# Kernel tuning notes

Hardware: AMD Instinct MI355X
Metric: run time of the kernel (lower is better)

The kernel has to match this reference:

```python
import jax, jax.numpy as jnp
import numpy as np

NU, NM = 100000, 20000
E, EUU = 1000000, 500000
DU, DM, H = 64, 128, 128
BN_EPS = 1e-5


def _sage(x_src, x_dst, src, dst, Wl, bl, Wr):
    # PyG SAGEConv (mean aggr): lin_l(mean_j x_src[j]) + lin_r(x_dst)
    n_dst = x_dst.shape[0]
    msg = x_src[src]                                   # [E, H] gather
    agg = jax.ops.segment_sum(msg, dst, num_segments=n_dst)
    cnt = jax.ops.segment_sum(jnp.ones((dst.shape[0],), x_src.dtype), dst, num_segments=n_dst)
    agg = agg / jnp.maximum(cnt, 1.0)[:, None]
    return agg @ Wl + bl + x_dst @ Wr


def setup_inputs() -> dict:
    key = jax.random.key(0)
    ks = iter(jax.random.split(key, 40))
    s = 0.08  # weight scale for numerical stability
    d = {}
    d['user_feat'] = jax.random.normal(next(ks), (NU, DU), jnp.float32)
    d['movie_feat'] = jax.random.normal(next(ks), (NM, DM), jnp.float32)
    d['W_user'] = jax.random.normal(next(ks), (DU, H), jnp.float32) * s
    d['b_user'] = jnp.zeros((H,), jnp.float32)
    d['W_movie'] = jax.random.normal(next(ks), (DM, H), jnp.float32) * s
    d['b_movie'] = jnp.zeros((H,), jnp.float32)
    for name in ['u2m1', 'm2u1', 'u2m2', 'm2u2', 'u2u']:
        d[name + '_Wl'] = jax.random.normal(next(ks), (H, H), jnp.float32) * s
        d[name + '_bl'] = jnp.zeros((H,), jnp.float32)
        d[name + '_Wr'] = jax.random.normal(next(ks), (H, H), jnp.float32) * s
    d['p1_W'] = jax.random.normal(next(ks), (2 * H, H), jnp.float32) * s
    d['p1_b'] = jnp.zeros((H,), jnp.float32)
    d['bn_gamma'] = jnp.ones((H,), jnp.float32)
    d['bn_beta'] = jnp.zeros((H,), jnp.float32)
    d['bn_mean'] = jnp.zeros((H,), jnp.float32)
    d['bn_var'] = jax.random.uniform(next(ks), (H,), jnp.float32, 0.5, 1.5)
    d['p2_W'] = jax.random.normal(next(ks), (H, 1), jnp.float32) * s
    d['p2_b'] = jnp.zeros((1,), jnp.float32)
    d['rated_src'] = jax.random.randint(next(ks), (E,), 0, NU, jnp.int32)
    d['rated_dst'] = jax.random.randint(next(ks), (E,), 0, NM, jnp.int32)
    d['uu_src'] = jax.random.randint(next(ks), (EUU,), 0, NU, jnp.int32)
    d['uu_dst'] = jax.random.randint(next(ks), (EUU,), 0, NU, jnp.int32)
    return d


def reference(user_feat, movie_feat, W_user, b_user, W_movie, b_movie,
              u2m1_Wl, u2m1_bl, u2m1_Wr, m2u1_Wl, m2u1_bl, m2u1_Wr,
              u2m2_Wl, u2m2_bl, u2m2_Wr, m2u2_Wl, m2u2_bl, m2u2_Wr,
              u2u_Wl, u2u_bl, u2u_Wr,
              p1_W, p1_b, bn_gamma, bn_beta, bn_mean, bn_var, p2_W, p2_b,
              rated_src, rated_dst, uu_src, uu_dst):
    relu = jax.nn.relu
    ux = relu(user_feat @ W_user + b_user)     # [NU, H]
    mx = relu(movie_feat @ W_movie + b_movie)  # [NM, H]
    # user -> movie, movie -> user (reversed edges), twice
    mx = relu(_sage(ux, mx, rated_src, rated_dst, u2m1_Wl, u2m1_bl, u2m1_Wr))
    ux = relu(_sage(mx, ux, rated_dst, rated_src, m2u1_Wl, m2u1_bl, m2u1_Wr))
    mx = relu(_sage(ux, mx, rated_src, rated_dst, u2m2_Wl, u2m2_bl, u2m2_Wr))
    ux = relu(_sage(mx, ux, rated_dst, rated_src, m2u2_Wl, m2u2_bl, m2u2_Wr))
    # user -> user follows
    ux = relu(_sage(ux, ux, uu_src, uu_dst, u2u_Wl, u2u_bl, u2u_Wr))
    # edge embedding + MLP predictor (BN/Dropout in eval mode)
    emb = jnp.concatenate([ux[rated_src], mx[rated_dst]], axis=1)  # [E, 2H]
    h = emb @ p1_W + p1_b
    h = (h - bn_mean) * jax.lax.rsqrt(bn_var + BN_EPS) * bn_gamma + bn_beta
    h = relu(h)
    pred = jax.nn.sigmoid(h @ p2_W + p2_b)[:, 0]
    return pred * 4.0 + 1.0
```

## Files before the change

### kernel.cpp

```cpp
#include <hip/hip_runtime.h>
#include <cmath>


#define NUSR 100000
#define NMOV 20000
#define NEDG 1000000
#define NEUU 500000
#define DH 128

#define CAPM 96
#define CAPU 32
#define CAPUU 24

#define NBD 128
#define WD 157
#define NBS 128
#define WS 782
#define NBU 196
#define WU 512
#define NBT (NBD + NBS + NBU)

#define LCD 36
#define LCS 36
#define LCU 20
#define BKD 8448
#define BKS 8448
#define BKU 2944

#define NBINB 977
#define EPSL 32
#define NEPB (EPSL * 128)

#define GLU ((NUSR + 127) / 128)
#define GLM ((NMOV + 127) / 128)
#define GSU 512
#define GSM 157

typedef unsigned short ushort_t;
typedef unsigned char uchar_t;
typedef __attribute__((ext_vector_type(8))) short short8;
typedef __attribute__((ext_vector_type(4))) float f32x4;
typedef __attribute__((ext_vector_type(2))) float f32x2;

__device__ __forceinline__ ushort_t f2bf(float f) {
  unsigned u = __float_as_uint(f);
  u += 0x7FFFu + ((u >> 16) & 1u);
  return (ushort_t)(u >> 16);
}
__device__ __forceinline__ uchar_t f2fp8(float v) {
  return (uchar_t)(__builtin_amdgcn_cvt_pk_fp8_f32(v, v, 0, false) & 0xFF);
}
__device__ __forceinline__ void fp8x8_to_f32(uint2 v, float* f) {
  f32x2 a = __builtin_amdgcn_cvt_pk_f32_fp8((int)v.x, false);
  f32x2 b = __builtin_amdgcn_cvt_pk_f32_fp8((int)v.x, true);
  f32x2 c = __builtin_amdgcn_cvt_pk_f32_fp8((int)v.y, false);
  f32x2 d = __builtin_amdgcn_cvt_pk_f32_fp8((int)v.y, true);
  f[0] = a.x; f[1] = a.y; f[2] = b.x; f[3] = b.y;
  f[4] = c.x; f[5] = c.y; f[6] = d.x; f[7] = d.y;
}
__device__ __forceinline__ int ntl(const int* p) { return __builtin_nontemporal_load(p); }
__device__ __forceinline__ unsigned ntl(const unsigned* p) { return __builtin_nontemporal_load(p); }
__device__ __forceinline__ ushort_t ntl(const ushort_t* p) { return __builtin_nontemporal_load(p); }

struct PrepArgs {
  const float* Wl[6];
  const float* Wr[6];
};
__global__ __launch_bounds__(256) void prep_all_k(
    PrepArgs pa, ushort_t* __restrict__ Wt,
    const float* __restrict__ W_user, const float* __restrict__ W_movie,
    ushort_t* __restrict__ WtU, ushort_t* __restrict__ WtM,
    const float* __restrict__ p1b, const float* __restrict__ gamma,
    const float* __restrict__ beta, const float* __restrict__ mean,
    const float* __restrict__ var,
    float* __restrict__ SEP, float* __restrict__ TEP,
    int* __restrict__ bcnt)
{
  int blk = blockIdx.x;
  if (blk < 768) {
    int wi = blk >> 7;
    int idx = (blk & 127) * 256 + threadIdx.x;
    int n = idx >> 8, k = idx & 255;
    const float* Wl = pa.Wl[wi];
    const float* Wr = pa.Wr[wi];
    float v = (k < DH) ? Wl[k * DH + n] : Wr[(k - DH) * DH + n];
    Wt[(size_t)wi * 32768 + n * 256 + k] = f2bf(v);
  } else if (blk < 800) {
    int idx = (blk - 768) * 256 + threadIdx.x;
    int n = idx >> 6, k = idx & 63;
    WtU[n * 64 + k] = f2bf(W_user[k * DH + n]);
  } else if (blk < 864) {
    int idx = (blk - 800) * 256 + threadIdx.x;
    int n = idx >> 7, k = idx & 127;
    WtM[n * 128 + k] = f2bf(W_movie[k * DH + n]);
  } else {
    int f = threadIdx.x;
    if (f < DH) {
      float sc = gamma[f] * rsqrtf(var[f] + 1e-5f);
      SEP[f] = sc;
      TEP[f] = (p1b[f] - mean[f]) * sc + beta[f];
    }
    for (int i = threadIdx.x; i < NBT; i += 256) bcnt[i] = 0;
  }
}

__global__ __launch_bounds__(256) void bin_rated_k(
    const int* __restrict__ rsrc, const int* __restrict__ rdst,
    unsigned* __restrict__ bkt_d, uint2* __restrict__ bkt_s2,
    int* __restrict__ bcnt)
{
  __shared__ unsigned sb_d[NBD * LCD];
  __shared__ uint2 sb_s[NBS * LCS];
  __shared__ int lcnt[NBD + NBS];
  __shared__ int gbase[NBD + NBS];
  const int tid = threadIdx.x;
  for (int i = tid; i < NBD + NBS; i += 256) lcnt[i] = 0;
  __syncthreads();
  const int c = blockIdx.x;
#pragma unroll
  for (int it = 0; it < 4; ++it) {
    int e = c * 1024 + it * 256 + tid;
    if (e < NEDG) {
      int s = ntl(&rsrc[e]), d = ntl(&rdst[e]);
      int bd = d / WD;
      int o = atomicAdd(&lcnt[bd], 1);
      if (o < LCD) sb_d[bd * LCD + o] = (unsigned)(d - bd * WD) | ((unsigned)s << 8);
      int bs = s / WS;
      int o2 = atomicAdd(&lcnt[NBD + bs], 1);
      if (o2 < LCS)
        sb_s[bs * LCS + o2] =
            make_uint2((unsigned)(s - bs * WS) | ((unsigned)d << 10), (unsigned)e);
    }
  }
  __syncthreads();
  for (int i = tid; i < NBD + NBS; i += 256) {
    int n = lcnt[i];
    if (n > LCD) n = LCD;
    lcnt[i] = n;
    gbase[i] = atomicAdd(&bcnt[i], n);
  }
  __syncthreads();
  const int qw = tid >> 4, lq = tid & 15;
  for (int t = qw; t < NBD + NBS; t += 16) {
    int n = lcnt[t], gb = gbase[t];
    if (t < NBD) {
      if (gb + n > BKD) n = BKD - gb;
      unsigned* gp = bkt_d + (size_t)t * BKD;
      const unsigned* sp = sb_d + t * LCD;
      for (int i = lq; i < n; i += 16) gp[gb + i] = sp[i];
    } else {
      int b = t - NBD;
      if (gb + n > BKS) n = BKS - gb;
      uint2* gp = bkt_s2 + (size_t)b * BKS;
      const uint2* sp = sb_s + b * LCS;
      for (int i = lq; i < n; i += 16) gp[gb + i] = sp[i];
    }
  }
}

__global__ __launch_bounds__(256) void bin_uu_k(
    const int* __restrict__ usrc, const int* __restrict__ udst,
    unsigned* __restrict__ bkt_u, int* __restrict__ bcnt)
{
  __shared__ unsigned sb_u[NBU * LCU];
  __shared__ int lcnt[NBU];
  __shared__ int gbase[NBU];
  const int tid = threadIdx.x;
  for (int i = tid; i < NBU; i += 256) lcnt[i] = 0;
  __syncthreads();
  const int c = blockIdx.x;
#pragma unroll
  for (int it = 0; it < 2; ++it) {
    int e = c * 512 + it * 256 + tid;
    if (e < NEUU) {
      int s = ntl(&usrc[e]), d = ntl(&udst[e]);
      int bu = d >> 9;
      int o = atomicAdd(&lcnt[bu], 1);
      if (o < LCU) sb_u[bu * LCU + o] = (unsigned)(d & 511) | ((unsigned)s << 9);
    }
  }
  __syncthreads();
  for (int i = tid; i < NBU; i += 256) {
    int n = lcnt[i];
    if (n > LCU) n = LCU;
    lcnt[i] = n;
    gbase[i] = atomicAdd(&bcnt[NBD + NBS + i], n);
  }
  __syncthreads();
  const int qw = tid >> 4, lq = tid & 15;
  for (int t = qw; t < NBU; t += 16) {
    int n = lcnt[t], gb = gbase[t];
    if (gb + n > BKU) n = BKU - gb;
    unsigned* gp = bkt_u + (size_t)t * BKU;
    const unsigned* sp = sb_u + t * LCU;
    for (int i = lq; i < n; i += 16) gp[gb + i] = sp[i];
  }
}

__global__ __launch_bounds__(256) void csr_k(
    const unsigned* __restrict__ bkt_d, const uint2* __restrict__ bkt_s2,
    const unsigned* __restrict__ bkt_u, const int* __restrict__ bcnt,
    int* __restrict__ cnt_m, int* __restrict__ cnt_u, int* __restrict__ cnt_uu,
    int* __restrict__ col_m, ushort_t* __restrict__ col_u, int* __restrict__ col_uu)
{
  __shared__ int lc[WS];
  __shared__ alignas(16) unsigned cbuf[WD * CAPM];
  const int tid = threadIdx.x;
  const int bid = blockIdx.x;
  if (bid < NBD) {
    const int b = bid;
    const int nr = (NMOV - b * WD < WD) ? (NMOV - b * WD) : WD;
    for (int m = tid; m < nr; m += 256) lc[m] = 0;
    __syncthreads();
    int n = bcnt[b]; if (n > BKD) n = BKD;
    const unsigned* B = bkt_d + (size_t)b * BKD;
    for (int i = tid; i < n; i += 256) {
      unsigned v = ntl(&B[i]);
      int m = (int)(v & 255u);
      int o = atomicAdd(&lc[m], 1);
      if (o < CAPM) cbuf[m * CAPM + o] = v >> 8;
    }
    __syncthreads();
    for (int m = tid; m < nr; m += 256) cnt_m[b * WD + m] = lc[m];
    int4* dst = (int4*)(col_m + (size_t)b * WD * CAPM);
    const int4* src = (const int4*)cbuf;
    const int tot = nr * (CAPM / 4);
    for (int i = tid; i < tot; i += 256) dst[i] = src[i];
  } else if (bid < NBD + NBS) {
    const int b = bid - NBD;
    const int nr = (NUSR - b * WS < WS) ? (NUSR - b * WS) : WS;
    for (int u = tid; u < nr; u += 256) lc[u] = 0;
    __syncthreads();
    int n = bcnt[NBD + b]; if (n > BKS) n = BKS;
    const uint2* B = bkt_s2 + (size_t)b * BKS;
    ushort_t* cb16 = (ushort_t*)cbuf;
    for (int i = tid; i < n; i += 256) {
      unsigned v = B[i].x;
      int u = (int)(v & 1023u);
      int o = atomicAdd(&lc[u], 1);
      if (o < CAPU) cb16[u * CAPU + o] = (ushort_t)(v >> 10);
    }
    __syncthreads();
    for (int u = tid; u < nr; u += 256) cnt_u[b * WS + u] = lc[u];
    int4* dst = (int4*)(col_u + (size_t)b * WS * CAPU);
    const int4* src = (const int4*)cbuf;
    const int tot = nr * (CAPU / 8);
    for (int i = tid; i < tot; i += 256) dst[i] = src[i];
  } else {
    const int b = bid - NBD - NBS;
    const int nr = (NUSR - b * WU < WU) ? (NUSR - b * WU) : WU;
    for (int u = tid; u < nr; u += 256) lc[u] = 0;
    __syncthreads();
    int n = bcnt[NBD + NBS + b]; if (n > BKU) n = BKU;
    const unsigned* B = bkt_u + (size_t)b * BKU;
    for (int i = tid; i < n; i += 256) {
      unsigned v = ntl(&B[i]);
      int u = (int)(v & 511u);
      int o = atomicAdd(&lc[u], 1);
      if (o < CAPUU) cbuf[u * CAPUU + o] = v >> 9;
    }
    __syncthreads();
    for (int u = tid; u < nr; u += 256) cnt_uu[b * WU + u] = lc[u];
    int4* dst = (int4*)(col_uu + (size_t)b * WU * CAPUU);
    const int4* src = (const int4*)cbuf;
    const int tot = nr * (CAPUU / 4);
    for (int i = tid; i < tot; i += 256) dst[i] = src[i];
  }
}

template <int K>
__device__ __forceinline__ void lin_body(
    int lblk, const float* __restrict__ X, const ushort_t* __restrict__ Wt,
    const float* __restrict__ b, ushort_t* __restrict__ Y,
    uchar_t* __restrict__ Y8, int N)
{
  const int wave = threadIdx.x >> 6;
  const int lane = threadIdx.x & 63;
  const int row0 = (lblk * 4 + wave) * 32;
  if (row0 >= N) return;
  const int lm = lane & 15;
  const int koff = (lane >> 4) * 8;

  f32x4 acc[2][8];
#pragma unroll
  for (int a = 0; a < 2; ++a)
#pragma unroll
    for (int nt = 0; nt < 8; ++nt) acc[a][nt] = (f32x4){0.f, 0.f, 0.f, 0.f};

#pragma unroll
  for (int ks = 0; ks < K / 32; ++ks) {
    short8 af[2];
#pragma unroll
    for (int a = 0; a < 2; ++a) {
      const float* p = X + (size_t)(row0 + a * 16 + lm) * K + ks * 32 + koff;
      float4 v0 = *(const float4*)p;
      float4 v1 = *(const float4*)(p + 4);
      short8 s;
      s[0] = (short)f2bf(v0.x); s[1] = (short)f2bf(v0.y);
      s[2] = (short)f2bf(v0.z); s[3] = (short)f2bf(v0.w);
      s[4] = (short)f2bf(v1.x); s[5] = (short)f2bf(v1.y);
      s[6] = (short)f2bf(v1.z); s[7] = (short)f2bf(v1.w);
      af[a] = s;
    }
#pragma unroll
    for (int nt = 0; nt < 8; ++nt) {
      short8 bf = *(const short8*)&Wt[(nt * 16 + lm) * K + ks * 32 + koff];
      acc[0][nt] = __builtin_amdgcn_mfma_f32_16x16x32_bf16(af[0], bf, acc[0][nt], 0, 0, 0);
      acc[1][nt] = __builtin_amdgcn_mfma_f32_16x16x32_bf16(af[1], bf, acc[1][nt], 0, 0, 0);
    }
  }

  const int quad = lane >> 4;
  float bv[8];
#pragma unroll
  for (int nt = 0; nt < 8; ++nt) bv[nt] = b[nt * 16 + lm];
#pragma unroll
  for (int a = 0; a < 2; ++a) {
#pragma unroll
    for (int reg = 0; reg < 4; ++reg) {
      const int r = row0 + a * 16 + quad * 4 + reg;
      float vv[8];
#pragma unroll
      for (int nt = 0; nt < 8; ++nt)
        vv[nt] = fmaxf(acc[a][nt][reg] + bv[nt], 0.f);
#pragma unroll
      for (int nt = 0; nt < 8; ++nt)
        Y[(size_t)r * DH + nt * 16 + lm] = f2bf(vv[nt]);
#pragma unroll
      for (int nt = 0; nt < 8; ++nt)
        Y8[(size_t)r * DH + nt * 16 + lm] = f2fp8(vv[nt]);
    }
  }
}

__global__ __launch_bounds__(256) void lin2_k(
    const float* __restrict__ user_feat, const ushort_t* __restrict__ WtU,
    const float* __restrict__ b_user, ushort_t* __restrict__ ux, uchar_t* __restrict__ ux8,
    const float* __restrict__ movie_feat, const ushort_t* __restrict__ WtM,
    const float* __restrict__ b_movie, ushort_t* __restrict__ mx, uchar_t* __restrict__ mx8)
{
  const int blk = blockIdx.x;
  if (blk < GLU) lin_body<64>(blk, user_feat, WtU, b_user, ux, ux8, NUSR);
  else lin_body<128>(blk - GLU, movie_feat, WtM, b_movie, mx, mx8, NMOV);
}

template <typename CT, int CAP, int UNR>
__global__ __launch_bounds__(256) void agg_mean4_k(
    const uchar_t* __restrict__ x8, const int* __restrict__ cnt,
    const CT* __restrict__ col, ushort_t* __restrict__ out, int N)
{
  const int wave = threadIdx.x >> 6;
  const int lane = threadIdx.x & 63;
  const int lm = lane & 15, q = lane >> 4;
  const int row = blockIdx.x * 16 + wave * 4 + q;
  if (row >= N) return;
  const int deg = cnt[row];
  const int e = (deg < CAP) ? deg : CAP;
  const CT* crow = col + (size_t)row * CAP;
  float a[8];
#pragma unroll
  for (int j = 0; j < 8; ++j) a[j] = 0.f;
  int i = 0;
  if (UNR >= 16) {
    for (; i + 15 < e; i += 16) {
      uint2 v[16];
#pragma unroll
      for (int u = 0; u < 16; ++u) {
        int s = (int)ntl(&crow[i + u]);
        v[u] = *(const uint2*)(x8 + (size_t)s * DH + lm * 8);
      }
#pragma unroll
      for (int u = 0; u < 16; ++u) {
        float f0[8];
        fp8x8_to_f32(v[u], f0);
#pragma unroll
        for (int j = 0; j < 8; ++j) a[j] += f0[j];
      }
    }
  }
  if (UNR >= 8) {
    for (; i + 7 < e; i += 8) {
      uint2 v[8];
#pragma unroll
      for (int u = 0; u < 8; ++u) {
        int s = (int)ntl(&crow[i + u]);
        v[u] = *(const uint2*)(x8 + (size_t)s * DH + lm * 8);
      }
#pragma unroll
      for (int u = 0; u < 8; ++u) {
        float f0[8];
        fp8x8_to_f32(v[u], f0);
#pragma unroll
        for (int j = 0; j < 8; ++j) a[j] += f0[j];
      }
    }
  }
  for (; i + 3 < e; i += 4) {
    uint2 v0, v1, v2, v3;
    int s0 = (int)ntl(&crow[i]), s1 = (int)ntl(&crow[i + 1]);
    int s2 = (int)ntl(&crow[i + 2]), s3 = (int)ntl(&crow[i + 3]);
    v0 = *(const uint2*)(x8 + (size_t)s0 * DH + lm * 8);
    v1 = *(const uint2*)(x8 + (size_t)s1 * DH + lm * 8);
    v2 = *(const uint2*)(x8 + (size_t)s2 * DH + lm * 8);
    v3 = *(const uint2*)(x8 + (size_t)s3 * DH + lm * 8);
    float f0[8], f1[8], f2[8], f3[8];
    fp8x8_to_f32(v0, f0); fp8x8_to_f32(v1, f1);
    fp8x8_to_f32(v2, f2); fp8x8_to_f32(v3, f3);
#pragma unroll
    for (int j = 0; j < 8; ++j) a[j] += (f0[j] + f1[j]) + (f2[j] + f3[j]);
  }
  for (; i < e; ++i) {
    uint2 v0 = *(const uint2*)(x8 + (size_t)(int)ntl(&crow[i]) * DH + lm * 8);
    float f0[8];
    fp8x8_to_f32(v0, f0);
#pragma unroll
    for (int j = 0; j < 8; ++j) a[j] += f0[j];
  }
  float inv = 1.f / (float)(deg > 1 ? deg : 1);
  unsigned p0 = f2bf(a[0] * inv) | ((unsigned)f2bf(a[1] * inv) << 16);
  unsigned p1 = f2bf(a[2] * inv) | ((unsigned)f2bf(a[3] * inv) << 16);
  unsigned p2 = f2bf(a[4] * inv) | ((unsigned)f2bf(a[5] * inv) << 16);
  unsigned p3 = f2bf(a[6] * inv) | ((unsigned)f2bf(a[7] * inv) << 16);
  *(int4*)(out + (size_t)row * DH + lm * 8) = make_int4(p0, p1, p2, p3);
}

__global__ __launch_bounds__(256) void sage_mfma_k(
    const ushort_t* __restrict__ A0, const ushort_t* __restrict__ A1,
    const ushort_t* __restrict__ Wt, const float* __restrict__ bl,
    ushort_t* __restrict__ out, uchar_t* __restrict__ out8, int N)
{
  __shared__ alignas(16) ushort_t WtS[32768];
  const int tid = threadIdx.x;
  for (int f = tid; f < 4096; f += 256) {
    const int r = f >> 5, c = f & 31;
    const int4 v = *(const int4*)(Wt + (size_t)f * 8);
    *(int4*)&WtS[(size_t)((r << 5) | (c ^ (r & 31))) << 3] = v;
  }
  __syncthreads();

  const int wave = tid >> 6;
  const int lane = tid & 63;
  const int lm = lane & 15;
  const int kq = lane >> 4;
  const int koff = kq * 8;
  const int quad = kq;

  float bv[8];
#pragma unroll
  for (int nt = 0; nt < 8; ++nt) bv[nt] = bl[nt * 16 + lm];

  const int T = (N + 31) >> 5;
  for (int t = (int)blockIdx.x * 4 + wave; t < T; t += (int)gridDim.x * 4) {
    const int row0 = t * 32;
    size_t abase[2];
#pragma unroll
    for (int a = 0; a < 2; ++a) abase[a] = (size_t)(row0 + a * 16 + lm) * DH;

    f32x4 acc[2][8];
#pragma unroll
    for (int a = 0; a < 2; ++a)
#pragma unroll
      for (int nt = 0; nt < 8; ++nt) acc[a][nt] = (f32x4){0.f, 0.f, 0.f, 0.f};

#pragma unroll
    for (int ks = 0; ks < 8; ++ks) {
      short8 af[2];
#pragma unroll
      for (int a = 0; a < 2; ++a) {
        const ushort_t* p = (ks < 4) ? (A0 + abase[a] + ks * 32 + koff)
                                     : (A1 + abase[a] + (ks - 4) * 32 + koff);
        af[a] = *(const short8*)p;
      }
#pragma unroll
      for (int nt = 0; nt < 8; ++nt) {
        const int r = nt * 16 + lm;
        const int c = (ks * 4 + kq) ^ (r & 31);
        short8 bf = *(const short8*)&WtS[(size_t)((r << 5) | c) << 3];
        acc[0][nt] = __builtin_amdgcn_mfma_f32_16x16x32_bf16(af[0], bf, acc[0][nt], 0, 0, 0);
        acc[1][nt] = __builtin_amdgcn_mfma_f32_16x16x32_bf16(af[1], bf, acc[1][nt], 0, 0, 0);
      }
    }

#pragma unroll
    for (int a = 0; a < 2; ++a) {
#pragma unroll
      for (int reg = 0; reg < 4; ++reg) {
        const int r = row0 + a * 16 + quad * 4 + reg;
        float vv[8];
#pragma unroll
        for (int nt = 0; nt < 8; ++nt)
          vv[nt] = fmaxf(acc[a][nt][reg] + bv[nt], 0.f);
#pragma unroll
        for (int nt = 0; nt < 8; ++nt)
          out[(size_t)r * DH + nt * 16 + lm] = f2bf(vv[nt]);
        if (out8) {
#pragma unroll
          for (int nt = 0; nt < 8; ++nt)
            out8[(size_t)r * DH + nt * 16 + lm] = f2fp8(vv[nt]);
        }
      }
    }
  }
}

__device__ __forceinline__ void proj_body(
    int lblk, const ushort_t* __restrict__ A, const ushort_t* __restrict__ Wt,
    int kofs, ushort_t* __restrict__ out, int N)
{
  const int wave = threadIdx.x >> 6;
  const int lane = threadIdx.x & 63;
  const int row0 = (lblk * 4 + wave) * 32;
  if (row0 >= N) return;
  const int lm = lane & 15;
  const int koff = (lane >> 4) * 8;

  size_t abase[2];
#pragma unroll
  for (int a = 0; a < 2; ++a) abase[a] = (size_t)(row0 + a * 16 + lm) * DH;

  f32x4 acc[2][8];
#pragma unroll
  for (int a = 0; a < 2; ++a)
#pragma unroll
    for (int nt = 0; nt < 8; ++nt) acc[a][nt] = (f32x4){0.f, 0.f, 0.f, 0.f};

#pragma unroll
  for (int ks = 0; ks < 4; ++ks) {
    short8 af[2];
#pragma unroll
    for (int a = 0; a < 2; ++a) af[a] = *(const short8*)(A + abase[a] + ks * 32 + koff);
#pragma unroll
    for (int nt = 0; nt < 8; ++nt) {
      short8 bf = *(const short8*)&Wt[(nt * 16 + lm) * 256 + kofs + ks * 32 + koff];
      acc[0][nt] = __builtin_amdgcn_mfma_f32_16x16x32_bf16(af[0], bf, acc[0][nt], 0, 0, 0);
      acc[1][nt] = __builtin_amdgcn_mfma_f32_16x16x32_bf16(af[1], bf, acc[1][nt], 0, 0, 0);
    }
  }

  const int quad = lane >> 4;
#pragma unroll
  for (int a = 0; a < 2; ++a) {
#pragma unroll
    for (int reg = 0; reg < 4; ++reg) {
      const int r = row0 + a * 16 + quad * 4 + reg;
#pragma unroll
      for (int nt = 0; nt < 8; ++nt)
        out[(size_t)r * DH + nt * 16 + lm] = f2bf(acc[a][nt][reg]);
    }
  }
}

__global__ __launch_bounds__(256) void proj2_k(
    const ushort_t* __restrict__ ux, const ushort_t* __restrict__ mx,
    const ushort_t* __restrict__ Wt, ushort_t* __restrict__ pu,
    ushort_t* __restrict__ pm, int gmU)
{
  if ((int)blockIdx.x < gmU) proj_body(blockIdx.x, ux, Wt, 0, pu, NUSR);
  else proj_body(blockIdx.x - gmU, mx, Wt, DH, pm, NMOV);
}

__global__ __launch_bounds__(256) void ep_bkt_k(
    const ushort_t* __restrict__ pu, const ushort_t* __restrict__ pm,
    const uint2* __restrict__ bkt_s2, const int* __restrict__ bcnt,
    const float* __restrict__ SEP, const float* __restrict__ TEP,
    const float* __restrict__ p2W, const float* __restrict__ p2b,
    float* __restrict__ out)
{
  const int b = (int)blockIdx.x & 127;
  const int sl = (int)blockIdx.x >> 7;
  const int tid = threadIdx.x;
  const int lm = tid & 15;
  const int qw = tid >> 4;
  const int f0 = lm * 8;

  float S[8], T8[8], w2[8];
#pragma unroll
  for (int j = 0; j < 8; ++j) {
    S[j] = SEP[f0 + j];
    T8[j] = TEP[f0 + j];
    w2[j] = p2W[f0 + j];
  }
  const float bias2 = p2b[0];

  int n = bcnt[NBD + b];
  if (n > BKS) n = BKS;
  const uint2* B = bkt_s2 + (size_t)b * BKS;
  const int ub = b * WS;
  const int chunk = (n + EPSL - 1) / EPSL;
  const int st = sl * chunk;
  int en = st + chunk;
  if (en > n) en = n;

  for (int i = st + qw; i < en; i += 32) {
    const int i2 = i + 16;
    const bool v2 = (i2 < en);
    uint2 e0 = B[i];
    uint2 e1 = v2 ? B[i2] : e0;
    int s0 = ub + (int)(e0.x & 1023u), d0 = (int)(e0.x >> 10);
    int s1 = ub + (int)(e1.x & 1023u), d1 = (int)(e1.x >> 10);
    int4 uv0 = *(const int4*)(pu + (s0 << 7) + f0);
    int4 mv0 = *(const int4*)(pm + (d0 << 7) + f0);
    int4 uv1 = *(const int4*)(pu + (s1 << 7) + f0);
    int4 mv1 = *(const int4*)(pm + (d1 << 7) + f0);
    float fu0[8], fm0[8], fu1[8], fm1[8];
    {
      unsigned a0 = (unsigned)uv0.x, b0 = (unsigned)uv0.y, c0 = (unsigned)uv0.z, dd0 = (unsigned)uv0.w;
      fu0[0] = __uint_as_float(a0 << 16); fu0[1] = __uint_as_float(a0 & 0xFFFF0000u);
      fu0[2] = __uint_as_float(b0 << 16); fu0[3] = __uint_as_float(b0 & 0xFFFF0000u);
      fu0[4] = __uint_as_float(c0 << 16); fu0[5] = __uint_as_float(c0 & 0xFFFF0000u);
      fu0[6] = __uint_as_float(dd0 << 16); fu0[7] = __uint_as_float(dd0 & 0xFFFF0000u);
      unsigned a1 = (unsigned)mv0.x, b1 = (unsigned)mv0.y, c1 = (unsigned)mv0.z, dd1 = (unsigned)mv0.w;
      fm0[0] = __uint_as_float(a1 << 16); fm0[1] = __uint_as_float(a1 & 0xFFFF0000u);
      fm0[2] = __uint_as_float(b1 << 16); fm0[3] = __uint_as_float(b1 & 0xFFFF0000u);
      fm0[4] = __uint_as_float(c1 << 16); fm0[5] = __uint_as_float(c1 & 0xFFFF0000u);
      fm0[6] = __uint_as_float(dd1 << 16); fm0[7] = __uint_as_float(dd1 & 0xFFFF0000u);
      unsigned a2 = (unsigned)uv1.x, b2 = (unsigned)uv1.y, c2 = (unsigned)uv1.z, dd2 = (unsigned)uv1.w;
      fu1[0] = __uint_as_float(a2 << 16); fu1[1] = __uint_as_float(a2 & 0xFFFF0000u);
      fu1[2] = __uint_as_float(b2 << 16); fu1[3] = __uint_as_float(b2 & 0xFFFF0000u);
      fu1[4] = __uint_as_float(c2 << 16); fu1[5] = __uint_as_float(c2 & 0xFFFF0000u);
      fu1[6] = __uint_as_float(dd2 << 16); fu1[7] = __uint_as_float(dd2 & 0xFFFF0000u);
      unsigned a3 = (unsigned)mv1.x, b3 = (unsigned)mv1.y, c3 = (unsigned)mv1.z, dd3 = (unsigned)mv1.w;
      fm1[0] = __uint_as_float(a3 << 16); fm1[1] = __uint_as_float(a3 & 0xFFFF0000u);
      fm1[2] = __uint_as_float(b3 << 16); fm1[3] = __uint_as_float(b3 & 0xFFFF0000u);
      fm1[4] = __uint_as_float(c3 << 16); fm1[5] = __uint_as_float(c3 & 0xFFFF0000u);
      fm1[6] = __uint_as_float(dd3 << 16); fm1[7] = __uint_as_float(dd3 & 0xFFFF0000u);
    }
    float p0 = 0.f, p1 = 0.f;
#pragma unroll
    for (int j = 0; j < 8; ++j) {
      float h0 = fmaxf(fmaf(fu0[j] + fm0[j], S[j], T8[j]), 0.f);
      p0 = fmaf(h0, w2[j], p0);
      float h1 = fmaxf(fmaf(fu1[j] + fm1[j], S[j], T8[j]), 0.f);
      p1 = fmaf(h1, w2[j], p1);
    }
    p0 += __shfl_xor(p0, 1, 16);
    p0 += __shfl_xor(p0, 2, 16);
    p0 += __shfl_xor(p0, 4, 16);
    p0 += __shfl_xor(p0, 8, 16);
    p1 += __shfl_xor(p1, 1, 16);
    p1 += __shfl_xor(p1, 2, 16);
    p1 += __shfl_xor(p1, 4, 16);
    p1 += __shfl_xor(p1, 8, 16);
    if (lm == 0) {
      __builtin_nontemporal_store(4.f / (1.f + expf(-(p0 + bias2))) + 1.f, &out[e0.y]);
      if (v2)
        __builtin_nontemporal_store(4.f / (1.f + expf(-(p1 + bias2))) + 1.f, &out[e1.y]);
    }
  }
}

extern "C" void kernel_launch(void* const* d_in, const int* in_sizes, int n_in,
                              void* d_out, int out_size, void* d_ws, size_t ws_size,
                              hipStream_t stream)
{
  const float* user_feat = (const float*)d_in[0];
  const float* movie_feat = (const float*)d_in[1];
  const float* W_user = (const float*)d_in[2];
  const float* b_user = (const float*)d_in[3];
  const float* W_movie = (const float*)d_in[4];
  const float* b_movie = (const float*)d_in[5];
  const float* u2m1_Wl = (const float*)d_in[6];
  const float* u2m1_bl = (const float*)d_in[7];
  const float* u2m1_Wr = (const float*)d_in[8];
  const float* m2u1_Wl = (const float*)d_in[9];
  const float* m2u1_bl = (const float*)d_in[10];
  const float* m2u1_Wr = (const float*)d_in[11];
  const float* u2m2_Wl = (const float*)d_in[12];
  const float* u2m2_bl = (const float*)d_in[13];
  const float* u2m2_Wr = (const float*)d_in[14];
  const float* m2u2_Wl = (const float*)d_in[15];
  const float* m2u2_bl = (const float*)d_in[16];
  const float* m2u2_Wr = (const float*)d_in[17];
  const float* u2u_Wl = (const float*)d_in[18];
  const float* u2u_bl = (const float*)d_in[19];
  const float* u2u_Wr = (const float*)d_in[20];
  const float* p1_W = (const float*)d_in[21];
  const float* p1_b = (const float*)d_in[22];
  const float* bn_gamma = (const float*)d_in[23];
  const float* bn_beta = (const float*)d_in[24];
  const float* bn_mean = (const float*)d_in[25];
  const float* bn_var = (const float*)d_in[26];
  const float* p2_W = (const float*)d_in[27];
  const float* p2_b = (const float*)d_in[28];
  const int* rated_src = (const int*)d_in[29];
  const int* rated_dst = (const int*)d_in[30];
  const int* uu_src = (const int*)d_in[31];
  const int* uu_dst = (const int*)d_in[32];

  ushort_t* ux = (ushort_t*)d_ws;
  ushort_t* mx = ux + (size_t)NUSR * DH;
  ushort_t* agg = mx + (size_t)NMOV * DH;
  ushort_t* pm = agg + (size_t)NUSR * DH;
  ushort_t* Wt = pm + (size_t)NMOV * DH;
  ushort_t* WtU = Wt + 6 * 32768;
  ushort_t* WtM = WtU + 8192;
  float* SEP = (float*)(WtM + 16384);
  float* TEP = SEP + DH;
  int* col_m = (int*)(TEP + DH);
  ushort_t* col_u = (ushort_t*)(col_m + (size_t)NMOV * CAPM);
  int* col_uu = (int*)(col_u + (size_t)NUSR * CAPU);
  int* cntbuf = col_uu + (size_t)NUSR * CAPUU;
  uchar_t* ux8 = (uchar_t*)(cntbuf + (NMOV + 2 * NUSR + NBT));
  uchar_t* mx8 = ux8 + (size_t)NUSR * DH;
  uint2* bkt_s2 = (uint2*)(mx8 + (size_t)NMOV * DH);
  int* cnt_m = cntbuf;
  int* cnt_u = cntbuf + NMOV;
  int* cnt_uu = cntbuf + NMOV + NUSR;
  int* bcnt = cntbuf + NMOV + 2 * NUSR;

  unsigned* bkt_d = (unsigned*)agg;
  unsigned* bkt_u = bkt_d + (size_t)NBD * BKD;

  ushort_t* Wt_u2m1 = Wt + 0 * 32768;
  ushort_t* Wt_m2u1 = Wt + 1 * 32768;
  ushort_t* Wt_u2m2 = Wt + 2 * 32768;
  ushort_t* Wt_m2u2 = Wt + 3 * 32768;
  ushort_t* Wt_u2u  = Wt + 4 * 32768;
  ushort_t* Wt_p1   = Wt + 5 * 32768;
  ushort_t* pu = agg;

  PrepArgs pa;
  pa.Wl[0] = u2m1_Wl; pa.Wr[0] = u2m1_Wr;
  pa.Wl[1] = m2u1_Wl; pa.Wr[1] = m2u1_Wr;
  pa.Wl[2] = u2m2_Wl; pa.Wr[2] = u2m2_Wr;
  pa.Wl[3] = m2u2_Wl; pa.Wr[3] = m2u2_Wr;
  pa.Wl[4] = u2u_Wl;  pa.Wr[4] = u2u_Wr;
  pa.Wl[5] = p1_W;    pa.Wr[5] = p1_W + DH * DH;
  prep_all_k<<<865, 256, 0, stream>>>(
      pa, Wt, W_user, W_movie, WtU, WtM,
      p1_b, bn_gamma, bn_beta, bn_mean, bn_var, SEP, TEP, bcnt);

  bin_rated_k<<<NBINB, 256, 0, stream>>>(
      rated_src, rated_dst, bkt_d, bkt_s2, bcnt);
  bin_uu_k<<<NBINB, 256, 0, stream>>>(uu_src, uu_dst, bkt_u, bcnt);
  csr_k<<<NBT, 256, 0, stream>>>(
      bkt_d, bkt_s2, bkt_u, bcnt, cnt_m, cnt_u, cnt_uu, col_m, col_u, col_uu);
  lin2_k<<<GLU + GLM, 256, 0, stream>>>(
      user_feat, WtU, b_user, ux, ux8, movie_feat, WtM, b_movie, mx, mx8);

  const int gaM = (NMOV + 15) / 16, gaU = (NUSR + 15) / 16;
  agg_mean4_k<int, CAPM, 16><<<gaM, 256, 0, stream>>>(ux8, cnt_m, col_m, agg, NMOV);
  sage_mfma_k<<<GSM, 256, 0, stream>>>(agg, mx, Wt_u2m1, u2m1_bl, mx, mx8, NMOV);
  agg_mean4_k<ushort_t, CAPU, 8><<<gaU, 256, 0, stream>>>(mx8, cnt_u, col_u, agg, NUSR);
  sage_mfma_k<<<GSU, 256, 0, stream>>>(agg, ux, Wt_m2u1, m2u1_bl, ux, ux8, NUSR);
  agg_mean4_k<int, CAPM, 16><<<gaM, 256, 0, stream>>>(ux8, cnt_m, col_m, agg, NMOV);
  sage_mfma_k<<<GSM, 256, 0, stream>>>(agg, mx, Wt_u2m2, u2m2_bl, mx, mx8, NMOV);
  agg_mean4_k<ushort_t, CAPU, 8><<<gaU, 256, 0, stream>>>(mx8, cnt_u, col_u, agg, NUSR);
  sage_mfma_k<<<GSU, 256, 0, stream>>>(agg, ux, Wt_m2u2, m2u2_bl, ux, ux8, NUSR);
  agg_mean4_k<int, CAPUU, 8><<<gaU, 256, 0, stream>>>(ux8, cnt_uu, col_uu, agg, NUSR);
  sage_mfma_k<<<GSU, 256, 0, stream>>>(agg, ux, Wt_u2u, u2u_bl, ux, (uchar_t*)nullptr, NUSR);

  const int gmU = (NUSR + 127) / 128, gmM = (NMOV + 127) / 128;
  proj2_k<<<gmU + gmM, 256, 0, stream>>>(ux, mx, Wt_p1, pu, pm, gmU);
  ep_bkt_k<<<NEPB, 256, 0, stream>>>(
      pu, pm, bkt_s2, bcnt, SEP, TEP, p2_W, p2_b, (float*)d_out);
}
```

Before: 560.4 us.

## Fuse mean aggregation into SAGE MFMA kernel, removing intermediate agg buffer

Replaces the separate neighbor-mean gather kernel and the dense MFMA kernel with one kernel. Each wave gathers the fp8 neighbor rows for 16 destination rows, builds the bf16 A-fragment in registers, and multiplies it against the LDS-resident weights together with the self features. This removes the bf16 agg write and re-read plus one launch per layer. The trade-off is less gather parallelism, since each wave now handles 16 rows and each lane walks one row's edge list serially. That can cause load imbalance and fewer in-flight loads, especially for high-degree movie rows.

```diff
diff --git a/kernel.cpp b/kernel.cpp
--- a/kernel.cpp
+++ b/kernel.cpp
@@ -33,8 +33,8 @@
 
 #define GLU ((NUSR + 127) / 128)
 #define GLM ((NMOV + 127) / 128)
-#define GSU 512
-#define GSM 157
+#define GFU 512
+#define GFM 313
 
 typedef unsigned short ushort_t;
 typedef unsigned char uchar_t;
@@ -344,88 +344,10 @@
   else lin_body<128>(blk - GLU, movie_feat, WtM, b_movie, mx, mx8, NMOV);
 }
 
-template <typename CT, int CAP, int UNR>
-__global__ __launch_bounds__(256) void agg_mean4_k(
+template <typename CT, int CAP>
+__global__ __launch_bounds__(256) void fused_sage_k(
     const uchar_t* __restrict__ x8, const int* __restrict__ cnt,
-    const CT* __restrict__ col, ushort_t* __restrict__ out, int N)
-{
-  const int wave = threadIdx.x >> 6;
-  const int lane = threadIdx.x & 63;
-  const int lm = lane & 15, q = lane >> 4;
-  const int row = blockIdx.x * 16 + wave * 4 + q;
-  if (row >= N) return;
-  const int deg = cnt[row];
-  const int e = (deg < CAP) ? deg : CAP;
-  const CT* crow = col + (size_t)row * CAP;
-  float a[8];
-#pragma unroll
-  for (int j = 0; j < 8; ++j) a[j] = 0.f;
-  int i = 0;
-  if (UNR >= 16) {
-    for (; i + 15 < e; i += 16) {
-      uint2 v[16];
-#pragma unroll
-      for (int u = 0; u < 16; ++u) {
-        int s = (int)ntl(&crow[i + u]);
-        v[u] = *(const uint2*)(x8 + (size_t)s * DH + lm * 8);
-      }
-#pragma unroll
-      for (int u = 0; u < 16; ++u) {
-        float f0[8];
-        fp8x8_to_f32(v[u], f0);
-#pragma unroll
-        for (int j = 0; j < 8; ++j) a[j] += f0[j];
-      }
-    }
-  }
-  if (UNR >= 8) {
-    for (; i + 7 < e; i += 8) {
-      uint2 v[8];
-#pragma unroll
-      for (int u = 0; u < 8; ++u) {
-        int s = (int)ntl(&crow[i + u]);
-        v[u] = *(const uint2*)(x8 + (size_t)s * DH + lm * 8);
-      }
-#pragma unroll
-      for (int u = 0; u < 8; ++u) {
-        float f0[8];
-        fp8x8_to_f32(v[u], f0);
-#pragma unroll
-        for (int j = 0; j < 8; ++j) a[j] += f0[j];
-      }
-    }
-  }
-  for (; i + 3 < e; i += 4) {
-    uint2 v0, v1, v2, v3;
-    int s0 = (int)ntl(&crow[i]), s1 = (int)ntl(&crow[i + 1]);
-    int s2 = (int)ntl(&crow[i + 2]), s3 = (int)ntl(&crow[i + 3]);
-    v0 = *(const uint2*)(x8 + (size_t)s0 * DH + lm * 8);
-    v1 = *(const uint2*)(x8 + (size_t)s1 * DH + lm * 8);
-    v2 = *(const uint2*)(x8 + (size_t)s2 * DH + lm * 8);
-    v3 = *(const uint2*)(x8 + (size_t)s3 * DH + lm * 8);
-    float f0[8], f1[8], f2[8], f3[8];
-    fp8x8_to_f32(v0, f0); fp8x8_to_f32(v1, f1);
-    fp8x8_to_f32(v2, f2); fp8x8_to_f32(v3, f3);
-#pragma unroll
-    for (int j = 0; j < 8; ++j) a[j] += (f0[j] + f1[j]) + (f2[j] + f3[j]);
-  }
-  for (; i < e; ++i) {
-    uint2 v0 = *(const uint2*)(x8 + (size_t)(int)ntl(&crow[i]) * DH + lm * 8);
-    float f0[8];
-    fp8x8_to_f32(v0, f0);
-#pragma unroll
-    for (int j = 0; j < 8; ++j) a[j] += f0[j];
-  }
-  float inv = 1.f / (float)(deg > 1 ? deg : 1);
-  unsigned p0 = f2bf(a[0] * inv) | ((unsigned)f2bf(a[1] * inv) << 16);
-  unsigned p1 = f2bf(a[2] * inv) | ((unsigned)f2bf(a[3] * inv) << 16);
-  unsigned p2 = f2bf(a[4] * inv) | ((unsigned)f2bf(a[5] * inv) << 16);
-  unsigned p3 = f2bf(a[6] * inv) | ((unsigned)f2bf(a[7] * inv) << 16);
-  *(int4*)(out + (size_t)row * DH + lm * 8) = make_int4(p0, p1, p2, p3);
-}
-
-__global__ __launch_bounds__(256) void sage_mfma_k(
-    const ushort_t* __restrict__ A0, const ushort_t* __restrict__ A1,
+    const CT* __restrict__ col, const ushort_t* __restrict__ A1,
     const ushort_t* __restrict__ Wt, const float* __restrict__ bl,
     ushort_t* __restrict__ out, uchar_t* __restrict__ out8, int N)
 {
@@ -442,62 +364,112 @@
   const int lane = tid & 63;
   const int lm = lane & 15;
   const int kq = lane >> 4;
-  const int koff = kq * 8;
-  const int quad = kq;
 
   float bv[8];
 #pragma unroll
   for (int nt = 0; nt < 8; ++nt) bv[nt] = bl[nt * 16 + lm];
 
-  const int T = (N + 31) >> 5;
+  const int T = N >> 4;
   for (int t = (int)blockIdx.x * 4 + wave; t < T; t += (int)gridDim.x * 4) {
-    const int row0 = t * 32;
-    size_t abase[2];
-#pragma unroll
-    for (int a = 0; a < 2; ++a) abase[a] = (size_t)(row0 + a * 16 + lm) * DH;
-
-    f32x4 acc[2][8];
-#pragma unroll
-    for (int a = 0; a < 2; ++a)
-#pragma unroll
-      for (int nt = 0; nt < 8; ++nt) acc[a][nt] = (f32x4){0.f, 0.f, 0.f, 0.f};
-
-#pragma unroll
-    for (int ks = 0; ks < 8; ++ks) {
-      short8 af[2];
-#pragma unroll
-      for (int a = 0; a < 2; ++a) {
-        const ushort_t* p = (ks < 4) ? (A0 + abase[a] + ks * 32 + koff)
-                                     : (A1 + abase[a] + (ks - 4) * 32 + koff);
-        af[a] = *(const short8*)p;
+    const int row = t * 16 + lm;
+    const int deg = cnt[row];
+    const int e = (deg < CAP) ? deg : CAP;
+    const CT* crow = col + (size_t)row * CAP;
+    const uchar_t* xb = x8 + kq * 8;
+
+    float ac[4][8];
+#pragma unroll
+    for (int ks = 0; ks < 4; ++ks)
+#pragma unroll
+      for (int j = 0; j < 8; ++j) ac[ks][j] = 0.f;
+
+    int i = 0;
+    for (; i + 3 < e; i += 4) {
+      int s0 = (int)ntl(&crow[i]);
+      int s1 = (int)ntl(&crow[i + 1]);
+      int s2 = (int)ntl(&crow[i + 2]);
+      int s3 = (int)ntl(&crow[i + 3]);
+      uint2 v0[4], v1[4], v2[4], v3[4];
+#pragma unroll
+      for (int ks = 0; ks < 4; ++ks) {
+        v0[ks] = *(const uint2*)(xb + (size_t)s0 * DH + ks * 32);
+        v1[ks] = *(const uint2*)(xb + (size_t)s1 * DH + ks * 32);
+        v2[ks] = *(const uint2*)(xb + (size_t)s2 * DH + ks * 32);
+        v3[ks] = *(const uint2*)(xb + (size_t)s3 * DH + ks * 32);
       }
+#pragma unroll
+      for (int ks = 0; ks < 4; ++ks) {
+        float f0[8], f1[8], f2[8], f3[8];
+        fp8x8_to_f32(v0[ks], f0); fp8x8_to_f32(v1[ks], f1);
+        fp8x8_to_f32(v2[ks], f2); fp8x8_to_f32(v3[ks], f3);
+#pragma unroll
+        for (int j = 0; j < 8; ++j)
+          ac[ks][j] += (f0[j] + f1[j]) + (f2[j] + f3[j]);
+      }
+    }
+    for (; i < e; ++i) {
+      int s = (int)ntl(&crow[i]);
+#pragma unroll
+      for (int ks = 0; ks < 4; ++ks) {
+        uint2 v = *(const uint2*)(xb + (size_t)s * DH + ks * 32);
+        float f[8];
+        fp8x8_to_f32(v, f);
+#pragma unroll
+        for (int j = 0; j < 8; ++j) ac[ks][j] += f[j];
+      }
+    }
+
+    const float inv = 1.f / (float)(deg > 1 ? deg : 1);
+    short8 af[4];
+#pragma unroll
+    for (int ks = 0; ks < 4; ++ks) {
+      short8 s;
+#pragma unroll
+      for (int j = 0; j < 8; ++j) s[j] = (short)f2bf(ac[ks][j] * inv);
+      af[ks] = s;
+    }
+
+    f32x4 acc[8];
+#pragma unroll
+    for (int nt = 0; nt < 8; ++nt) acc[nt] = (f32x4){0.f, 0.f, 0.f, 0.f};
+
+#pragma unroll
+    for (int ks = 0; ks < 4; ++ks) {
 #pragma unroll
       for (int nt = 0; nt < 8; ++nt) {
         const int r = nt * 16 + lm;
         const int c = (ks * 4 + kq) ^ (r & 31);
         short8 bf = *(const short8*)&WtS[(size_t)((r << 5) | c) << 3];
-        acc[0][nt] = __builtin_amdgcn_mfma_f32_16x16x32_bf16(af[0], bf, acc[0][nt], 0, 0, 0);
-        acc[1][nt] = __builtin_amdgcn_mfma_f32_16x16x32_bf16(af[1], bf, acc[1][nt], 0, 0, 0);
+        acc[nt] = __builtin_amdgcn_mfma_f32_16x16x32_bf16(af[ks], bf, acc[nt], 0, 0, 0);
       }
     }
-
-#pragma unroll
-    for (int a = 0; a < 2; ++a) {
-#pragma unroll
-      for (int reg = 0; reg < 4; ++reg) {
-        const int r = row0 + a * 16 + quad * 4 + reg;
-        float vv[8];
+    const ushort_t* a1p = A1 + (size_t)row * DH + kq * 8;
+#pragma unroll
+    for (int ks = 4; ks < 8; ++ks) {
+      short8 afu = *(const short8*)(a1p + (ks - 4) * 32);
+#pragma unroll
+      for (int nt = 0; nt < 8; ++nt) {
+        const int r = nt * 16 + lm;
+        const int c = (ks * 4 + kq) ^ (r & 31);
+        short8 bf = *(const short8*)&WtS[(size_t)((r << 5) | c) << 3];
+        acc[nt] = __builtin_amdgcn_mfma_f32_16x16x32_bf16(afu, bf, acc[nt], 0, 0, 0);
+      }
+    }
+
+#pragma unroll
+    for (int reg = 0; reg < 4; ++reg) {
+      const int r = t * 16 + kq * 4 + reg;
+      float vv[8];
+#pragma unroll
+      for (int nt = 0; nt < 8; ++nt)
+        vv[nt] = fmaxf(acc[nt][reg] + bv[nt], 0.f);
+#pragma unroll
+      for (int nt = 0; nt < 8; ++nt)
+        out[(size_t)r * DH + nt * 16 + lm] = f2bf(vv[nt]);
+      if (out8) {
 #pragma unroll
         for (int nt = 0; nt < 8; ++nt)
-          vv[nt] = fmaxf(acc[a][nt][reg] + bv[nt], 0.f);
-#pragma unroll
-        for (int nt = 0; nt < 8; ++nt)
-          out[(size_t)r * DH + nt * 16 + lm] = f2bf(vv[nt]);
-        if (out8) {
-#pragma unroll
-          for (int nt = 0; nt < 8; ++nt)
-            out8[(size_t)r * DH + nt * 16 + lm] = f2fp8(vv[nt]);
-        }
+          out8[(size_t)r * DH + nt * 16 + lm] = f2fp8(vv[nt]);
       }
     }
   }
@@ -738,17 +710,16 @@
   lin2_k<<<GLU + GLM, 256, 0, stream>>>(
       user_feat, WtU, b_user, ux, ux8, movie_feat, WtM, b_movie, mx, mx8);
 
-  const int gaM = (NMOV + 15) / 16, gaU = (NUSR + 15) / 16;
-  agg_mean4_k<int, CAPM, 16><<<gaM, 256, 0, stream>>>(ux8, cnt_m, col_m, agg, NMOV);
-  sage_mfma_k<<<GSM, 256, 0, stream>>>(agg, mx, Wt_u2m1, u2m1_bl, mx, mx8, NMOV);
-  agg_mean4_k<ushort_t, CAPU, 8><<<gaU, 256, 0, stream>>>(mx8, cnt_u, col_u, agg, NUSR);
-  sage_mfma_k<<<GSU, 256, 0, stream>>>(agg, ux, Wt_m2u1, m2u1_bl, ux, ux8, NUSR);
-  agg_mean4_k<int, CAPM, 16><<<gaM, 256, 0, stream>>>(ux8, cnt_m, col_m, agg, NMOV);
-  sage_mfma_k<<<GSM, 256, 0, stream>>>(agg, mx, Wt_u2m2, u2m2_bl, mx, mx8, NMOV);
-  agg_mean4_k<ushort_t, CAPU, 8><<<gaU, 256, 0, stream>>>(mx8, cnt_u, col_u, agg, NUSR);
-  sage_mfma_k<<<GSU, 256, 0, stream>>>(agg, ux, Wt_m2u2, m2u2_bl, ux, ux8, NUSR);
-  agg_mean4_k<int, CAPUU, 8><<<gaU, 256, 0, stream>>>(ux8, cnt_uu, col_uu, agg, NUSR);
-  sage_mfma_k<<<GSU, 256, 0, stream>>>(agg, ux, Wt_u2u, u2u_bl, ux, (uchar_t*)nullptr, NUSR);
+  fused_sage_k<int, CAPM><<<GFM, 256, 0, stream>>>(
+      ux8, cnt_m, col_m, mx, Wt_u2m1, u2m1_bl, mx, mx8, NMOV);
+  fused_sage_k<ushort_t, CAPU><<<GFU, 256, 0, stream>>>(
+      mx8, cnt_u, col_u, ux, Wt_m2u1, m2u1_bl, ux, ux8, NUSR);
+  fused_sage_k<int, CAPM><<<GFM, 256, 0, stream>>>(
+      ux8, cnt_m, col_m, mx, Wt_u2m2, u2m2_bl, mx, mx8, NMOV);
+  fused_sage_k<ushort_t, CAPU><<<GFU, 256, 0, stream>>>(
+      mx8, cnt_u, col_u, ux, Wt_m2u2, m2u2_bl, ux, ux8, NUSR);
+  fused_sage_k<int, CAPUU><<<GFU, 256, 0, stream>>>(
+      ux8, cnt_uu, col_uu, ux, Wt_u2u, u2u_bl, ux, (uchar_t*)nullptr, NUSR);
 
   const int gmU = (NUSR + 127) / 128, gmM = (NMOV + 127) / 128;
   proj2_k<<<gmU + gmM, 256, 0, stream>>>(ux, mx, Wt_p1, pu, pm, gmU);
```

Measured after the change: 753.5 us. 34.5% more time.
